# Kernel optimization log

Measured on AMD Instinct MI355X. Metric: run time of the kernel, lower is better.

Reference implementation:

```python
import jax, jax.numpy as jnp
import numpy as np

N = 100000      # num nodes
E = 1600000     # num edges (avg degree 16)
ND = 32         # node_dim
ED = 32         # edge_dim
OD = 32         # out_dim


def setup_inputs() -> dict:
    key = jax.random.key(0)
    ks = jax.random.split(key, 7)
    node_x = jax.random.normal(ks[0], (N, ND), dtype=jnp.float32)
    edge_x = jax.random.normal(ks[1], (E, ED), dtype=jnp.float32)
    # forward() initializes g.ndata['z'] = torch.rand(N, node_dim+edge_dim)
    z_init = jax.random.uniform(ks[2], (N, ND + ED), dtype=jnp.float32)
    # pre_layer: Linear(ND+ED -> ND+ED); update_layer: Linear(2*ND+ED -> OD)
    W_pre = jax.random.normal(ks[3], (ND + ED, ND + ED), dtype=jnp.float32) / np.sqrt(ND + ED)
    b_pre = jnp.zeros((ND + ED,), dtype=jnp.float32)
    W_upd = jax.random.normal(ks[4], (2 * ND + ED, OD), dtype=jnp.float32) / np.sqrt(2 * ND + ED)
    b_upd = jnp.zeros((OD,), dtype=jnp.float32)
    src = jax.random.randint(ks[5], (E,), 0, N, dtype=jnp.int32)
    dst = jax.random.randint(ks[6], (E,), 0, N, dtype=jnp.int32)
    return {"node_x": node_x, "edge_x": edge_x, "z_init": z_init,
            "W_pre": W_pre, "b_pre": b_pre, "W_upd": W_upd, "b_upd": b_upd,
            "src": src, "dst": dst}


def reference(node_x, edge_x, z_init, W_pre, b_pre, W_upd, b_upd, src, dst):
    n = node_x.shape[0]
    # msg_func: per-edge gather + concat + Linear. Messages depend only on the
    # STATIC node feature 'x', so DGL's topological propagation is equivalent
    # to one edge-parallel pass.
    msg = jnp.concatenate([node_x[src], edge_x], axis=1) @ W_pre + b_pre  # [E, ND+ED]
    # reduce_func: sum over mailbox + ReLU (only fires for nodes with in-edges;
    # nodes with no incoming edges keep the random z_init).
    agg = jax.ops.segment_sum(msg, dst, num_segments=n)                    # [N, ND+ED]
    deg = jax.ops.segment_sum(jnp.ones_like(dst, dtype=node_x.dtype), dst, num_segments=n)
    z = jnp.where((deg > 0)[:, None], jax.nn.relu(agg), z_init)           # [N, ND+ED]
    # node_update: concat + Linear + ReLU
    h = jax.nn.relu(jnp.concatenate([node_x, z], axis=1) @ W_upd + b_upd)  # [N, OD]
    return h
```

## Files before the change

kernel.cpp:

```cpp
#include <hip/hip_runtime.h>


#define N_NODES 100000
#define N_EDGES 1600000
#define ND 32
#define ED 32
#define OD 32
#define ZD 64
#define NTILE 98

__device__ inline float bcast(float v, int lane) {
    return __uint_as_float(__builtin_amdgcn_readlane(__float_as_uint(v), lane));
}

__global__ __launch_bounds__(256) void hist8(const int* __restrict__ dst,
                                             int* __restrict__ h8) {
    int e = blockIdx.x * 256 + threadIdx.x;
    if (e < N_EDGES)
        atomicAdd(&h8[(blockIdx.x & 7) * N_NODES + dst[e]], 1);
}

__global__ __launch_bounds__(256) void reduce8(const int* __restrict__ h8,
                                               int* __restrict__ cnt) {
    int n = blockIdx.x * 256 + threadIdx.x;
    if (n < N_NODES) {
        int s = 0;
        #pragma unroll
        for (int x = 0; x < 8; ++x) s += h8[x * N_NODES + n];
        cnt[n] = s;
    }
}

__global__ __launch_bounds__(1024) void scan_part(const int* __restrict__ cnt,
                                                  int* __restrict__ part) {
    __shared__ int s[1024];
    int i = blockIdx.x * 1024 + threadIdx.x;
    s[threadIdx.x] = (i < N_NODES) ? cnt[i] : 0;
    __syncthreads();
    for (int off = 512; off > 0; off >>= 1) {
        if (threadIdx.x < off) s[threadIdx.x] += s[threadIdx.x + off];
        __syncthreads();
    }
    if (threadIdx.x == 0) part[blockIdx.x] = s[0];
}

__global__ void scan_top(int* part) {
    __shared__ int s[128];
    int v = (threadIdx.x < NTILE) ? part[threadIdx.x] : 0;
    s[threadIdx.x] = v;
    __syncthreads();
    for (int off = 1; off < 128; off <<= 1) {
        int u = (threadIdx.x >= off) ? s[threadIdx.x - off] : 0;
        __syncthreads();
        s[threadIdx.x] += u;
        __syncthreads();
    }
    if (threadIdx.x < NTILE) part[threadIdx.x] = s[threadIdx.x] - v;
}

__global__ __launch_bounds__(1024) void scan_local(const int* __restrict__ cnt,
                                                   const int* __restrict__ part,
                                                   int* __restrict__ cursor) {
    __shared__ int s[1024];
    int i = blockIdx.x * 1024 + threadIdx.x;
    int v = (i < N_NODES) ? cnt[i] : 0;
    s[threadIdx.x] = v;
    __syncthreads();
    for (int off = 1; off < 1024; off <<= 1) {
        int u = (threadIdx.x >= off) ? s[threadIdx.x - off] : 0;
        __syncthreads();
        s[threadIdx.x] += u;
        __syncthreads();
    }
    if (i < N_NODES) cursor[i] = part[blockIdx.x] + s[threadIdx.x] - v;
}

__global__ __launch_bounds__(256) void build_cur8(const int* __restrict__ h8,
                                                  const int* __restrict__ cursor,
                                                  int* __restrict__ c8) {
    int n = blockIdx.x * 256 + threadIdx.x;
    if (n < N_NODES) {
        int run = cursor[n];
        #pragma unroll
        for (int x = 0; x < 8; ++x) {
            c8[x * N_NODES + n] = run;
            run += h8[x * N_NODES + n];
        }
    }
}

__global__ __launch_bounds__(256) void permute_ids(
    const int* __restrict__ src, const int* __restrict__ dst,
    int* __restrict__ c8, int2* __restrict__ pair)
{
    int e = blockIdx.x * 256 + threadIdx.x;
    if (e >= N_EDGES) return;
    int pos = atomicAdd(&c8[(blockIdx.x & 7) * N_NODES + dst[e]], 1);
    pair[pos] = make_int2(src[e], e);
}

__global__ __launch_bounds__(256, 1) void z_csr(
    const float* __restrict__ node_x, const float* __restrict__ edge_x,
    const float* __restrict__ z_init,
    const float* __restrict__ W_pre, const float* __restrict__ b_pre,
    const int* __restrict__ cnt, const int* __restrict__ cursor,
    const int2* __restrict__ pair, float* __restrict__ zbuf)
{
    const int l = threadIdx.x & 63;
    float Wp[ZD];
    #pragma unroll
    for (int k = 0; k < ZD; ++k) Wp[k] = W_pre[k * ZD + l];
    const float bp = b_pre[l];
    const float* __restrict__ gbase = (l < ND) ? node_x : (edge_x - ND);

    int w  = (blockIdx.x * 256 + threadIdx.x) >> 6;
    int nw = (gridDim.x * 256) >> 6;
    for (int n = w; n < N_NODES; n += nw) {
        int dg = cnt[n];
        float z;
        if (dg > 0) {
            int j = cursor[n];
            int end = j + dg;
            float acc = 0.0f;
            for (; j + 8 <= end; j += 8) {
                int2 p0 = pair[j],   p1 = pair[j+1], p2 = pair[j+2], p3 = pair[j+3];
                int2 p4 = pair[j+4], p5 = pair[j+5], p6 = pair[j+6], p7 = pair[j+7];
                int s0 = (l < ND) ? p0.x : p0.y;
                int s1 = (l < ND) ? p1.x : p1.y;
                int s2 = (l < ND) ? p2.x : p2.y;
                int s3 = (l < ND) ? p3.x : p3.y;
                int s4 = (l < ND) ? p4.x : p4.y;
                int s5 = (l < ND) ? p5.x : p5.y;
                int s6 = (l < ND) ? p6.x : p6.y;
                int s7 = (l < ND) ? p7.x : p7.y;
                float v0 = gbase[(unsigned)s0 * 32u + (unsigned)l];
                float v1 = gbase[(unsigned)s1 * 32u + (unsigned)l];
                float v2 = gbase[(unsigned)s2 * 32u + (unsigned)l];
                float v3 = gbase[(unsigned)s3 * 32u + (unsigned)l];
                float v4 = gbase[(unsigned)s4 * 32u + (unsigned)l];
                float v5 = gbase[(unsigned)s5 * 32u + (unsigned)l];
                float v6 = gbase[(unsigned)s6 * 32u + (unsigned)l];
                float v7 = gbase[(unsigned)s7 * 32u + (unsigned)l];
                acc += ((v0 + v1) + (v2 + v3)) + ((v4 + v5) + (v6 + v7));
            }
            for (; j < end; ++j) {
                int2 p0 = pair[j];
                int s0 = (l < ND) ? p0.x : p0.y;
                acc += gbase[(unsigned)s0 * 32u + (unsigned)l];
            }
            float a0 = (float)dg * bp, a1 = 0.0f;
            #pragma unroll
            for (int k = 0; k < ZD; k += 2) {
                a0 += bcast(acc, k)     * Wp[k];
                a1 += bcast(acc, k + 1) * Wp[k + 1];
            }
            z = fmaxf(a0 + a1, 0.0f);
        } else {
            z = z_init[(long)n * ZD + l];
        }
        zbuf[(long)n * ZD + l] = z;
    }
}

__global__ __launch_bounds__(256) void edge_scatter(
    const float* __restrict__ node_x, const float* __restrict__ edge_x,
    const int* __restrict__ src, const int* __restrict__ dst,
    float* __restrict__ S, int* __restrict__ degI)
{
    long t = (long)blockIdx.x * 256 + threadIdx.x;
    int e = (int)(t >> 6), l = (int)(t & 63);
    if (e >= N_EDGES) return;
    int s = src[e], d = dst[e];
    float v = (l < ND) ? node_x[(long)s * ND + l] : edge_x[(long)e * ED + (l - ND)];
    atomicAdd(&S[(long)d * ZD + l], v);
    if (l == 0) atomicAdd(&degI[d], 1);
}

__global__ __launch_bounds__(256, 1) void z_dense(
    const float* __restrict__ z_init,
    const float* __restrict__ W_pre, const float* __restrict__ b_pre,
    float* __restrict__ S, const int* __restrict__ degI)
{
    const int l = threadIdx.x & 63;
    float Wp[ZD];
    #pragma unroll
    for (int k = 0; k < ZD; ++k) Wp[k] = W_pre[k * ZD + l];
    const float bp = b_pre[l];
    int w  = (blockIdx.x * 256 + threadIdx.x) >> 6;
    int nw = (gridDim.x * 256) >> 6;
    for (int n = w; n < N_NODES; n += nw) {
        int dg = degI[n];
        float sv = S[(long)n * ZD + l];
        float z;
        if (dg > 0) {
            float a0 = (float)dg * bp, a1 = 0.0f;
            #pragma unroll
            for (int k = 0; k < ZD; k += 2) {
                a0 += bcast(sv, k)     * Wp[k];
                a1 += bcast(sv, k + 1) * Wp[k + 1];
            }
            z = fmaxf(a0 + a1, 0.0f);
        } else {
            z = z_init[(long)n * ZD + l];
        }
        S[(long)n * ZD + l] = z;
    }
}

__global__ __launch_bounds__(256, 1) void h_upd(
    const float* __restrict__ node_x,
    const float* __restrict__ W_upd, const float* __restrict__ b_upd,
    const float* __restrict__ zbuf, float* __restrict__ out)
{
    const int l = threadIdx.x & 63;
    const int c = l & 31;
    float Wu[ND + ZD];
    #pragma unroll
    for (int k = 0; k < ND + ZD; ++k) Wu[k] = W_upd[k * OD + c];
    const float bu = b_upd[c];
    int w  = (blockIdx.x * 256 + threadIdx.x) >> 6;
    int nw = (gridDim.x * 256) >> 6;
    for (int n = w; n < N_NODES; n += nw) {
        float zv = zbuf[(long)n * ZD + l];
        float xv = node_x[(long)n * ND + c];
        float h0 = bu, h1 = 0.0f;
        #pragma unroll
        for (int k = 0; k < ND; k += 2) {
            h0 += bcast(xv, k)     * Wu[k];
            h1 += bcast(xv, k + 1) * Wu[k + 1];
        }
        #pragma unroll
        for (int k = 0; k < ZD; k += 2) {
            h0 += bcast(zv, k)     * Wu[ND + k];
            h1 += bcast(zv, k + 1) * Wu[ND + k + 1];
        }
        if (l < OD) out[(long)n * OD + l] = fmaxf(h0 + h1, 0.0f);
    }
}

extern "C" void kernel_launch(void* const* d_in, const int* in_sizes, int n_in,
                              void* d_out, int out_size, void* d_ws, size_t ws_size,
                              hipStream_t stream)
{
    const float* node_x = (const float*)d_in[0];
    const float* edge_x = (const float*)d_in[1];
    const float* z_init = (const float*)d_in[2];
    const float* W_pre  = (const float*)d_in[3];
    const float* b_pre  = (const float*)d_in[4];
    const float* W_upd  = (const float*)d_in[5];
    const float* b_upd  = (const float*)d_in[6];
    const int*   src    = (const int*)d_in[7];
    const int*   dst    = (const int*)d_in[8];
    float* out = (float*)d_out;

    size_t need = (size_t)N_EDGES * sizeof(int2)
                + (size_t)N_NODES * ZD * sizeof(float)
                + ((size_t)18 * N_NODES + 128) * sizeof(int);

    if (ws_size >= need) {
        int2*  pair   = (int2*)d_ws;
        float* zbuf   = (float*)(pair + N_EDGES);
        int*   cnt    = (int*)(zbuf + (size_t)N_NODES * ZD);
        int*   part   = cnt + N_NODES;
        int*   cursor = part + 128;
        int*   h8     = cursor + N_NODES;
        int*   c8     = h8 + 8 * N_NODES;

        (void)hipMemsetAsync(h8, 0, 8 * N_NODES * sizeof(int), stream);
        hist8<<<(N_EDGES + 255) / 256, 256, 0, stream>>>(dst, h8);
        reduce8<<<(N_NODES + 255) / 256, 256, 0, stream>>>(h8, cnt);
        scan_part<<<NTILE, 1024, 0, stream>>>(cnt, part);
        scan_top<<<1, 128, 0, stream>>>(part);
        scan_local<<<NTILE, 1024, 0, stream>>>(cnt, part, cursor);
        build_cur8<<<(N_NODES + 255) / 256, 256, 0, stream>>>(h8, cursor, c8);
        permute_ids<<<(N_EDGES + 255) / 256, 256, 0, stream>>>(src, dst, c8, pair);
        z_csr<<<2048, 256, 0, stream>>>(node_x, edge_x, z_init, W_pre, b_pre,
                                        cnt, cursor, pair, zbuf);
        h_upd<<<2048, 256, 0, stream>>>(node_x, W_upd, b_upd, zbuf, out);
    } else {
        float* S    = (float*)d_ws;
        int*   degI = (int*)(S + (size_t)N_NODES * ZD);
        (void)hipMemsetAsync(d_ws, 0,
            ((size_t)N_NODES * ZD + N_NODES) * sizeof(float), stream);
        edge_scatter<<<(int)(((long)N_EDGES * 64 + 255) / 256), 256, 0, stream>>>(
            node_x, edge_x, src, dst, S, degI);
        z_dense<<<2048, 256, 0, stream>>>(z_init, W_pre, b_pre, S, degI);
        h_upd<<<2048, 256, 0, stream>>>(node_x, W_upd, b_upd, S, out);
    }
}
```

Before: 680.8 us.

## Balance z_csr by edge count with binary search; fuse count/cursor helper kernels

The z_csr kernel now gives each wavefront a fixed slice of 128 edge slots. It finds its node range by binary-searching the cursor array, instead of striding over nodes. Degrees now come from adjacent cursor entries. This evens out work across waves with skewed degrees, at the cost of two binary searches per wave, more waves each loading W_pre, and a larger grid. Separately, the reduce8 and build_cur8 kernels are folded into scan_part and scan_local, which removes two launches and one pass over the count and cursor arrays.

```diff
diff --git a/kernel.cpp b/kernel.cpp
--- a/kernel.cpp
+++ b/kernel.cpp
@@ -8,6 +8,8 @@
 #define OD 32
 #define ZD 64
 #define NTILE 98
+#define SLOTS 128
+#define NWAVE (N_EDGES / SLOTS + 1)
 
 __device__ inline float bcast(float v, int lane) {
     return __uint_as_float(__builtin_amdgcn_readlane(__float_as_uint(v), lane));
@@ -20,22 +22,18 @@
         atomicAdd(&h8[(blockIdx.x & 7) * N_NODES + dst[e]], 1);
 }
 
-__global__ __launch_bounds__(256) void reduce8(const int* __restrict__ h8,
-                                               int* __restrict__ cnt) {
-    int n = blockIdx.x * 256 + threadIdx.x;
-    if (n < N_NODES) {
-        int s = 0;
-        #pragma unroll
-        for (int x = 0; x < 8; ++x) s += h8[x * N_NODES + n];
-        cnt[n] = s;
-    }
-}
-
-__global__ __launch_bounds__(1024) void scan_part(const int* __restrict__ cnt,
+__global__ __launch_bounds__(1024) void scan_part(const int* __restrict__ h8,
+                                                  int* __restrict__ cnt,
                                                   int* __restrict__ part) {
     __shared__ int s[1024];
     int i = blockIdx.x * 1024 + threadIdx.x;
-    s[threadIdx.x] = (i < N_NODES) ? cnt[i] : 0;
+    int v = 0;
+    if (i < N_NODES) {
+        #pragma unroll
+        for (int x = 0; x < 8; ++x) v += h8[x * N_NODES + i];
+        cnt[i] = v;
+    }
+    s[threadIdx.x] = v;
     __syncthreads();
     for (int off = 512; off > 0; off >>= 1) {
         if (threadIdx.x < off) s[threadIdx.x] += s[threadIdx.x + off];
@@ -60,7 +58,9 @@
 
 __global__ __launch_bounds__(1024) void scan_local(const int* __restrict__ cnt,
                                                    const int* __restrict__ part,
-                                                   int* __restrict__ cursor) {
+                                                   const int* __restrict__ h8,
+                                                   int* __restrict__ cursor,
+                                                   int* __restrict__ c8) {
     __shared__ int s[1024];
     int i = blockIdx.x * 1024 + threadIdx.x;
     int v = (i < N_NODES) ? cnt[i] : 0;
@@ -72,19 +72,13 @@
         s[threadIdx.x] += u;
         __syncthreads();
     }
-    if (i < N_NODES) cursor[i] = part[blockIdx.x] + s[threadIdx.x] - v;
-}
-
-__global__ __launch_bounds__(256) void build_cur8(const int* __restrict__ h8,
-                                                  const int* __restrict__ cursor,
-                                                  int* __restrict__ c8) {
-    int n = blockIdx.x * 256 + threadIdx.x;
-    if (n < N_NODES) {
-        int run = cursor[n];
+    if (i < N_NODES) {
+        int run = part[blockIdx.x] + s[threadIdx.x] - v;
+        cursor[i] = run;
         #pragma unroll
         for (int x = 0; x < 8; ++x) {
-            c8[x * N_NODES + n] = run;
-            run += h8[x * N_NODES + n];
+            c8[x * N_NODES + i] = run;
+            run += h8[x * N_NODES + i];
         }
     }
 }
@@ -99,11 +93,20 @@
     pair[pos] = make_int2(src[e], e);
 }
 
+__device__ inline int lbound(const int* __restrict__ cur, int x) {
+    int lo = 0, hi = N_NODES;
+    while (lo < hi) {
+        int mid = (lo + hi) >> 1;
+        if (cur[mid] < x) lo = mid + 1; else hi = mid;
+    }
+    return lo;
+}
+
 __global__ __launch_bounds__(256, 1) void z_csr(
     const float* __restrict__ node_x, const float* __restrict__ edge_x,
     const float* __restrict__ z_init,
     const float* __restrict__ W_pre, const float* __restrict__ b_pre,
-    const int* __restrict__ cnt, const int* __restrict__ cursor,
+    const int* __restrict__ cursor,
     const int2* __restrict__ pair, float* __restrict__ zbuf)
 {
     const int l = threadIdx.x & 63;
@@ -113,14 +116,18 @@
     const float bp = b_pre[l];
     const float* __restrict__ gbase = (l < ND) ? node_x : (edge_x - ND);
 
-    int w  = (blockIdx.x * 256 + threadIdx.x) >> 6;
-    int nw = (gridDim.x * 256) >> 6;
-    for (int n = w; n < N_NODES; n += nw) {
-        int dg = cnt[n];
+    int w = ((blockIdx.x * 256 + threadIdx.x) >> 6);
+    if (w >= NWAVE) return;
+    int lo = w * SLOTS;
+    int n0 = lbound(cursor, lo);
+    int n1 = lbound(cursor, lo + SLOTS);
+
+    for (int n = n0; n < n1; ++n) {
+        int j   = cursor[n];
+        int end = (n + 1 < N_NODES) ? cursor[n + 1] : N_EDGES;
+        int dg  = end - j;
         float z;
         if (dg > 0) {
-            int j = cursor[n];
-            int end = j + dg;
             float acc = 0.0f;
             for (; j + 8 <= end; j += 8) {
                 int2 p0 = pair[j],   p1 = pair[j+1], p2 = pair[j+2], p3 = pair[j+3];
@@ -268,14 +275,12 @@
 
         (void)hipMemsetAsync(h8, 0, 8 * N_NODES * sizeof(int), stream);
         hist8<<<(N_EDGES + 255) / 256, 256, 0, stream>>>(dst, h8);
-        reduce8<<<(N_NODES + 255) / 256, 256, 0, stream>>>(h8, cnt);
-        scan_part<<<NTILE, 1024, 0, stream>>>(cnt, part);
+        scan_part<<<NTILE, 1024, 0, stream>>>(h8, cnt, part);
         scan_top<<<1, 128, 0, stream>>>(part);
-        scan_local<<<NTILE, 1024, 0, stream>>>(cnt, part, cursor);
-        build_cur8<<<(N_NODES + 255) / 256, 256, 0, stream>>>(h8, cursor, c8);
+        scan_local<<<NTILE, 1024, 0, stream>>>(cnt, part, h8, cursor, c8);
         permute_ids<<<(N_EDGES + 255) / 256, 256, 0, stream>>>(src, dst, c8, pair);
-        z_csr<<<2048, 256, 0, stream>>>(node_x, edge_x, z_init, W_pre, b_pre,
-                                        cnt, cursor, pair, zbuf);
+        z_csr<<<(NWAVE * 64 + 255) / 256, 256, 0, stream>>>(
+            node_x, edge_x, z_init, W_pre, b_pre, cursor, pair, zbuf);
         h_upd<<<2048, 256, 0, stream>>>(node_x, W_upd, b_upd, zbuf, out);
     } else {
         float* S    = (float*)d_ws;
```

After: 721.5 us. 1.06x slower.
